# Kernel optimization log

Measured on AMD Instinct MI355X. Metric: run time of the kernel, lower is better.

The kernel has to match this reference:

```python
import jax, jax.numpy as jnp
import numpy as np

NH, WS, SS = 8, 7, 3  # num_heads, window_size, shift_size
EPS = 1e-5


def _rel_pos_index(ws):
    coords = np.stack(np.meshgrid(np.arange(ws), np.arange(ws), indexing='ij'))
    coords = coords.reshape(2, -1)                      # [2, L]
    rel = coords[:, :, None] - coords[:, None, :]       # [2, L, L]
    rel = rel.transpose(1, 2, 0) + (ws - 1)
    return rel[..., 0] * (2 * ws - 1) + rel[..., 1]     # [L, L] int


def _attn_mask(H, W, ws, ss):
    # region labels for shifted-window masking (torchvision semantics)
    img = np.zeros((H, W))
    slices = (slice(0, -ws), slice(-ws, -ss), slice(-ss, None))
    cnt = 0
    for hs in slices:
        for wsl in slices:
            img[hs, wsl] = cnt
            cnt += 1
    win = img.reshape(H // ws, ws, W // ws, ws).transpose(0, 2, 1, 3).reshape(-1, ws * ws)
    mask = (win[:, None, :] != win[:, :, None]).astype(np.float32) * (-100.0)
    return mask  # [nWin, L, L]


def _layernorm(x, gamma, beta):
    mu = jnp.mean(x, axis=-1, keepdims=True)
    var = jnp.mean(jnp.square(x - mu), axis=-1, keepdims=True)
    return (x - mu) * jax.lax.rsqrt(var + EPS) * gamma + beta


def _swin_attention(x, qkv_w, qkv_b, proj_w, proj_b, rpb_table):
    B, H, W, C = x.shape
    HD = C // NH
    L = WS * WS
    nH, nW = H // WS, W // WS
    # cyclic shift
    xs = jnp.roll(x, shift=(-SS, -SS), axis=(1, 2))
    # window partition -> [B*nWin, L, C]
    xw = xs.reshape(B, nH, WS, nW, WS, C).transpose(0, 1, 3, 2, 4, 5).reshape(B * nH * nW, L, C)
    qkv = jnp.einsum('nlc,dc->nld', xw, qkv_w) + qkv_b
    qkv = qkv.reshape(-1, L, 3, NH, HD).transpose(2, 0, 3, 1, 4)  # [3, N, h, L, d]
    q, k, v = qkv[0] * (HD ** -0.5), qkv[1], qkv[2]
    attn = jnp.einsum('nhid,nhjd->nhij', q, k)  # [N, h, L, L]
    bias = rpb_table[jnp.asarray(_rel_pos_index(WS))]  # [L, L, h]
    attn = attn + bias.transpose(2, 0, 1)[None]
    mask = jnp.asarray(_attn_mask(H, W, WS, SS))  # [nWin, L, L]
    nwin = nH * nW
    attn = attn.reshape(B, nwin, NH, L, L) + mask[None, :, None]
    attn = jax.nn.softmax(attn.reshape(-1, NH, L, L), axis=-1)
    out = jnp.einsum('nhij,nhjd->nhid', attn, v).transpose(0, 2, 1, 3).reshape(-1, L, C)
    out = jnp.einsum('nlc,dc->nld', out, proj_w) + proj_b
    # reverse windows and shift
    out = out.reshape(B, nH, nW, WS, WS, C).transpose(0, 1, 3, 2, 4, 5).reshape(B, H, W, C)
    return jnp.roll(out, shift=(SS, SS), axis=(1, 2))


def setup_inputs() -> dict:
    key = jax.random.key(0)
    ks = jax.random.split(key, 8)
    B, H, W, C = 32, 56, 56, 256
    F = 4 * C
    s = 0.02
    return {
        'x': jax.random.normal(ks[0], (B, H, W, C), jnp.float32),
        'qkv_w': jax.random.normal(ks[1], (3 * C, C), jnp.float32) * s,
        'qkv_b': jnp.zeros((3 * C,), jnp.float32),
        'proj_w': jax.random.normal(ks[2], (C, C), jnp.float32) * s,
        'proj_b': jnp.zeros((C,), jnp.float32),
        'rpb_table': jax.random.normal(ks[3], ((2 * WS - 1) ** 2, NH), jnp.float32) * s,
        'gamma1': jnp.ones((C,), jnp.float32),
        'beta1': jnp.zeros((C,), jnp.float32),
        'w1': jax.random.normal(ks[4], (C, F), jnp.float32) * s,
        'b1': jax.random.normal(ks[5], (F,), jnp.float32) * 1e-6,
        'w2': jax.random.normal(ks[6], (F, C), jnp.float32) * s,
        'b2': jax.random.normal(ks[7], (C,), jnp.float32) * 1e-6,
        'gamma2': jnp.ones((C,), jnp.float32),
        'beta2': jnp.zeros((C,), jnp.float32),
    }


def reference(x, qkv_w, qkv_b, proj_w, proj_b, rpb_table, gamma1, beta1, w1, b1, w2, b2, gamma2, beta2):
    # post-norm residual block: x + norm1(attn(x)); x + norm2(mlp(x))
    a = _swin_attention(x, qkv_w, qkv_b, proj_w, proj_b, rpb_table)
    x = x + _layernorm(a, gamma1, beta1)
    h = jax.nn.gelu(jnp.einsum('bhwc,cf->bhwf', x, w1) + b1, approximate=False)
    m = jnp.einsum('bhwf,fc->bhwc', h, w2) + b2
    x = x + _layernorm(m, gamma2, beta2)
    return x
```

## Files before the change

### kernel.cpp

```cpp
#include <hip/hip_runtime.h>
#include <hip/hip_bf16.h>


typedef unsigned short ushort_t;
typedef short bf16x8 __attribute__((ext_vector_type(8)));
typedef float f32x4 __attribute__((ext_vector_type(4)));

#define WAITV0 asm volatile("s_waitcnt vmcnt(0)" ::: "memory")
#define BAR    __builtin_amdgcn_s_barrier()

__device__ __forceinline__ float bf2f(unsigned short u) {
    union { unsigned int i; float f; } x; x.i = ((unsigned int)u) << 16; return x.f;
}
__device__ __forceinline__ unsigned short f2bf(float f) {
    union { float f; unsigned int i; } x; x.f = f;
    unsigned int r = x.i + 0x7fffu + ((x.i >> 16) & 1u);
    return (unsigned short)(r >> 16);
}
__device__ __forceinline__ bf16x8 pack8(float4 a, float4 b) {
    bf16x8 r;
    r[0] = (short)f2bf(a.x); r[1] = (short)f2bf(a.y);
    r[2] = (short)f2bf(a.z); r[3] = (short)f2bf(a.w);
    r[4] = (short)f2bf(b.x); r[5] = (short)f2bf(b.y);
    r[6] = (short)f2bf(b.z); r[7] = (short)f2bf(b.w);
    return r;
}
__device__ __forceinline__ void gl_lds16(const ushort_t* g, ushort_t* l) {
    __builtin_amdgcn_global_load_lds((const __attribute__((address_space(1))) void*)g,
                                     (__attribute__((address_space(3))) void*)l, 16, 0, 0);
}
__device__ __forceinline__ float gelu_f(float v) {
    float s = v * 0.70710678118654752f;
    float ax = fabsf(s);
    float t = __builtin_amdgcn_rcpf(1.0f + 0.3275911f * ax);
    float poly = ((((1.061405429f * t - 1.453152027f) * t + 1.421413741f) * t
                   - 0.284496736f) * t + 0.254829592f) * t;
    float y = 1.0f - poly * __expf(-ax * ax);
    float e = (s < 0.f) ? -y : y;
    return 0.5f * v * (1.0f + e);
}

__device__ __forceinline__ long swin_src_off(int m) {
    int n = m / 49, l = m - n * 49;
    int b = n >> 6, win = n & 63;
    int wh = win >> 3, ww = win & 7;
    int i = l / 7, j = l - i * 7;
    int hs = wh * 7 + i + 3; if (hs >= 56) hs -= 56;
    int ws = ww * 7 + j + 3; if (ws >= 56) ws -= 56;
    return ((long)(b * 56 + hs) * 56 + ws) * 256;
}

__global__ __launch_bounds__(256)
void xgather(const float* __restrict__ x, ushort_t* __restrict__ xg)
{
    int t = blockIdx.x * 256 + threadIdx.x;
    int row = t >> 5, ch = (t & 31) * 8;
    const float* src = x + swin_src_off(row) + ch;
    *(bf16x8*)(xg + (long)row * 256 + ch) = pack8(*(const float4*)src, *(const float4*)(src + 4));
}

template<int SRCT>
__global__ __launch_bounds__(256)
void convW(const float* __restrict__ src, ushort_t* __restrict__ dst, int N, int kshift)
{
    int idx = blockIdx.x * 256 + threadIdx.x;
    int kk = idx & ((1 << kshift) - 1), nn = idx >> kshift;
    float v = SRCT ? src[(long)kk * N + nn] : src[idx];
    dst[idx] = f2bf(v);
}

template<int ACT, int NCOLS>
__global__ __launch_bounds__(256)
void gemm128(const ushort_t* __restrict__ A, const ushort_t* __restrict__ W,
             const float* __restrict__ bias, ushort_t* __restrict__ C,
             int M, int N, int K)
{
    __shared__ ushort_t As[2][128 * 32];
    __shared__ ushort_t Bs[2][128 * 32];
    const int t = threadIdx.x, lane = t & 63, wave = t >> 6;
    const int cpx = gridDim.x >> 3;
    const int wg = (blockIdx.x & 7) * cpx + (blockIdx.x >> 3);
    const int row0 = (wg / NCOLS) * 128, col0 = (wg % NCOLS) * 128;
    const int wm = (wave >> 1) * 64, wn = (wave & 1) * 64;

    const int u0 = t, u1 = t + 256;
    const int r0 = u0 >> 2, s0 = ((u0 & 3) ^ ((r0 >> 1) & 3)) * 8;
    const int r1 = u1 >> 2, s1 = ((u1 & 3) ^ ((r1 >> 1) & 3)) * 8;
    const ushort_t* a0 = A + (long)(row0 + r0) * K + s0;
    const ushort_t* a1 = A + (long)(row0 + r1) * K + s1;
    const ushort_t* b0 = W + (long)(col0 + r0) * K + s0;
    const ushort_t* b1 = W + (long)(col0 + r1) * K + s1;

    int offA[4], offB[4];
    #pragma unroll
    for (int i = 0; i < 4; i++) {
        int ra = wm + i * 16 + (lane & 15);
        offA[i] = ra * 32 + (((lane >> 4) ^ ((ra >> 1) & 3)) * 8);
        int rb = wn + i * 16 + (lane & 15);
        offB[i] = rb * 32 + (((lane >> 4) ^ ((rb >> 1) & 3)) * 8);
    }

    f32x4 acc[4][4] = {};
    gl_lds16(a0, &As[0][u0 * 8]); gl_lds16(a1, &As[0][u1 * 8]);
    gl_lds16(b0, &Bs[0][u0 * 8]); gl_lds16(b1, &Bs[0][u1 * 8]);
    WAITV0; BAR;
    const int nk = K >> 5;
    for (int kt = 0; kt < nk - 1; kt++) {
        const int cur = kt & 1, nxt = cur ^ 1, k1 = (kt + 1) * 32;
        gl_lds16(a0 + k1, &As[nxt][u0 * 8]); gl_lds16(a1 + k1, &As[nxt][u1 * 8]);
        gl_lds16(b0 + k1, &Bs[nxt][u0 * 8]); gl_lds16(b1 + k1, &Bs[nxt][u1 * 8]);
        bf16x8 af[4], bw[4];
        #pragma unroll
        for (int i = 0; i < 4; i++) {
            af[i] = *(const bf16x8*)&As[cur][offA[i]];
            bw[i] = *(const bf16x8*)&Bs[cur][offB[i]];
        }
        #pragma unroll
        for (int mi = 0; mi < 4; mi++)
            #pragma unroll
            for (int ni = 0; ni < 4; ni++)
                acc[mi][ni] = __builtin_amdgcn_mfma_f32_16x16x32_bf16(af[mi], bw[ni], acc[mi][ni], 0, 0, 0);
        WAITV0; BAR;
    }
    {
        const int cur = (nk - 1) & 1;
        bf16x8 af[4], bw[4];
        #pragma unroll
        for (int i = 0; i < 4; i++) {
            af[i] = *(const bf16x8*)&As[cur][offA[i]];
            bw[i] = *(const bf16x8*)&Bs[cur][offB[i]];
        }
        #pragma unroll
        for (int mi = 0; mi < 4; mi++)
            #pragma unroll
            for (int ni = 0; ni < 4; ni++)
                acc[mi][ni] = __builtin_amdgcn_mfma_f32_16x16x32_bf16(af[mi], bw[ni], acc[mi][ni], 0, 0, 0);
    }
    #pragma unroll
    for (int mi = 0; mi < 4; mi++)
        #pragma unroll
        for (int ni = 0; ni < 4; ni++) {
            const int c = col0 + wn + ni * 16 + (lane & 15);
            const float bv = bias[c];
            #pragma unroll
            for (int r = 0; r < 4; r++) {
                const int rr = row0 + wm + mi * 16 + (lane >> 4) * 4 + r;
                float v = acc[mi][ni][r] + bv;
                if (ACT) v = gelu_f(v);
                C[(long)rr * N + c] = f2bf(v);
            }
        }
}

__global__ __launch_bounds__(64)
void attn_mfma(const ushort_t* __restrict__ qkv, const float* __restrict__ rpb,
               ushort_t* __restrict__ out)
{
    __shared__ ushort_t v_t[32 * 72];
    __shared__ ushort_t p_lds[64 * 72];
    __shared__ float bias_s[169];

    const int blk = blockIdx.x;
    const int n = blk >> 3, h = blk & 7;
    const int l = threadIdx.x;
    const long wbase = (long)n * 49 * 768 + h * 32;
    const float scale = 0.17677669529663687f;

    {
        int j = min(l, 48);
        const ushort_t* vr = qkv + wbase + (long)j * 768 + 512;
        #pragma unroll
        for (int c = 0; c < 4; c++) {
            bf16x8 vv = *(const bf16x8*)(vr + c * 8);
            #pragma unroll
            for (int e = 0; e < 8; e++) v_t[(c * 8 + e) * 72 + l] = (ushort_t)vv[e];
        }
    }
    for (int idx = l; idx < 169; idx += 64) bias_s[idx] = rpb[idx * 8 + h];
    __syncthreads();

    f32x4 s[4][4] = {};
    {
        bf16x8 aq[4], bk[4];
        #pragma unroll
        for (int mt = 0; mt < 4; mt++) {
            int i = min(mt * 16 + (l & 15), 48);
            aq[mt] = *(const bf16x8*)(qkv + wbase + (long)i * 768 + (l >> 4) * 8);
        }
        #pragma unroll
        for (int nt = 0; nt < 4; nt++) {
            int j = min(nt * 16 + (l & 15), 48);
            bk[nt] = *(const bf16x8*)(qkv + wbase + (long)j * 768 + 256 + (l >> 4) * 8);
        }
        #pragma unroll
        for (int mt = 0; mt < 4; mt++)
            #pragma unroll
            for (int nt = 0; nt < 4; nt++)
                s[mt][nt] = __builtin_amdgcn_mfma_f32_16x16x32_bf16(aq[mt], bk[nt], s[mt][nt], 0, 0, 0);
    }

    const int win = n & 63, wh = win >> 3, ww = win & 7;
    int yj[4], xj[4], regj[4]; bool jv[4];
    #pragma unroll
    for (int nt = 0; nt < 4; nt++) {
        int j = nt * 16 + (l & 15);
        jv[nt] = (j <= 48);
        int jc = min(j, 48);
        yj[nt] = jc / 7; xj[nt] = jc - yj[nt] * 7;
        int hs = wh * 7 + yj[nt], wsx = ww * 7 + xj[nt];
        regj[nt] = (hs < 49 ? 0 : (hs < 53 ? 1 : 2)) * 3 + (wsx < 49 ? 0 : (wsx < 53 ? 1 : 2));
    }
    float rinv[4][4];
    #pragma unroll
    for (int mt = 0; mt < 4; mt++) {
        #pragma unroll
        for (int r = 0; r < 4; r++) {
            int i = mt * 16 + (l >> 4) * 4 + r;
            int ic = min(i, 48);
            int yi = ic / 7, xi = ic - yi * 7;
            int hs = wh * 7 + yi, wsx = ww * 7 + xi;
            int regi = (hs < 49 ? 0 : (hs < 53 ? 1 : 2)) * 3 + (wsx < 49 ? 0 : (wsx < 53 ? 1 : 2));
            float val[4];
            #pragma unroll
            for (int nt = 0; nt < 4; nt++) {
                float v = s[mt][nt][r] * scale + bias_s[(yi - yj[nt] + 6) * 13 + (xi - xj[nt] + 6)];
                if (regi != regj[nt]) v -= 100.f;
                val[nt] = jv[nt] ? v : -1e30f;
            }
            float mx = fmaxf(fmaxf(val[0], val[1]), fmaxf(val[2], val[3]));
            #pragma unroll
            for (int off = 1; off <= 8; off <<= 1) mx = fmaxf(mx, __shfl_xor(mx, off));
            float sum = 0.f;
            #pragma unroll
            for (int nt = 0; nt < 4; nt++) { val[nt] = __expf(val[nt] - mx); sum += val[nt]; }
            #pragma unroll
            for (int off = 1; off <= 8; off <<= 1) sum += __shfl_xor(sum, off);
            rinv[mt][r] = 1.0f / sum;
            #pragma unroll
            for (int nt = 0; nt < 4; nt++)
                p_lds[i * 72 + nt * 16 + (l & 15)] = f2bf(val[nt]);
        }
    }
    __syncthreads();

    f32x4 o[4][2] = {};
    #pragma unroll
    for (int ks = 0; ks < 2; ks++) {
        bf16x8 pa[4], vb[2];
        #pragma unroll
        for (int mt = 0; mt < 4; mt++)
            pa[mt] = *(const bf16x8*)&p_lds[(mt * 16 + (l & 15)) * 72 + ks * 32 + (l >> 4) * 8];
        #pragma unroll
        for (int nt = 0; nt < 2; nt++)
            vb[nt] = *(const bf16x8*)&v_t[(nt * 16 + (l & 15)) * 72 + ks * 32 + (l >> 4) * 8];
        #pragma unroll
        for (int mt = 0; mt < 4; mt++)
            #pragma unroll
            for (int nt = 0; nt < 2; nt++)
                o[mt][nt] = __builtin_amdgcn_mfma_f32_16x16x32_bf16(pa[mt], vb[nt], o[mt][nt], 0, 0, 0);
    }
    #pragma unroll
    for (int mt = 0; mt < 4; mt++)
        #pragma unroll
        for (int r = 0; r < 4; r++) {
            int i = mt * 16 + (l >> 4) * 4 + r;
            if (i < 49) {
                float rs = rinv[mt][r];
                #pragma unroll
                for (int nt = 0; nt < 2; nt++) {
                    int d = nt * 16 + (l & 15);
                    out[((long)n * 49 + i) * 256 + h * 32 + d] = f2bf(o[mt][nt][r] * rs);
                }
            }
        }
}

__global__ __launch_bounds__(512)
void projln1(const ushort_t* __restrict__ A, const ushort_t* __restrict__ W,
             const float* __restrict__ pb, const float* __restrict__ x,
             const float* __restrict__ gamma, const float* __restrict__ beta,
             ushort_t* __restrict__ x1b)
{
    __shared__ ushort_t As[2][128 * 32];
    __shared__ ushort_t Bs[2][256 * 32];
    __shared__ float red_s[128][4];
    __shared__ float red_ss[128][4];
    __shared__ int srow_s[128];
    const int t = threadIdx.x, lane = t & 63, w = t >> 6;
    const int row0 = blockIdx.x * 128;
    const int wm = (w >> 2) * 64, wn = (w & 3) * 64;

    if (t < 128) srow_s[t] = (int)(swin_src_off(row0 + t) >> 8);

    const int ra0 = t >> 2, sa0 = ((t & 3) ^ ((ra0 >> 1) & 3)) * 8;
    const ushort_t* ag = A + (long)(row0 + ra0) * 256 + sa0;
    const int ub0 = t, ub1 = t + 512;
    const int rb0 = ub0 >> 2, sb0 = ((ub0 & 3) ^ ((rb0 >> 1) & 3)) * 8;
    const int rb1 = ub1 >> 2, sb1 = ((ub1 & 3) ^ ((rb1 >> 1) & 3)) * 8;
    const ushort_t* bg0 = W + (long)rb0 * 256 + sb0;
    const ushort_t* bg1 = W + (long)rb1 * 256 + sb1;

    int offA[4], offB[4];
    #pragma unroll
    for (int i = 0; i < 4; i++) {
        int ra = wm + i * 16 + (lane & 15);
        offA[i] = ra * 32 + (((lane >> 4) ^ ((ra >> 1) & 3)) * 8);
        int rb = wn + i * 16 + (lane & 15);
        offB[i] = rb * 32 + (((lane >> 4) ^ ((rb >> 1) & 3)) * 8);
    }

    f32x4 acc[4][4] = {};
    gl_lds16(ag, &As[0][t * 8]);
    gl_lds16(bg0, &Bs[0][ub0 * 8]); gl_lds16(bg1, &Bs[0][ub1 * 8]);
    WAITV0; BAR;
    for (int kt = 0; kt < 7; kt++) {
        const int cur = kt & 1, nxt = cur ^ 1, k1 = (kt + 1) * 32;
        gl_lds16(ag + k1, &As[nxt][t * 8]);
        gl_lds16(bg0 + k1, &Bs[nxt][ub0 * 8]); gl_lds16(bg1 + k1, &Bs[nxt][ub1 * 8]);
        bf16x8 af[4], bw[4];
        #pragma unroll
        for (int i = 0; i < 4; i++) {
            af[i] = *(const bf16x8*)&As[cur][offA[i]];
            bw[i] = *(const bf16x8*)&Bs[cur][offB[i]];
        }
        #pragma unroll
        for (int mi = 0; mi < 4; mi++)
            #pragma unroll
            for (int ni = 0; ni < 4; ni++)
                acc[mi][ni] = __builtin_amdgcn_mfma_f32_16x16x32_bf16(af[mi], bw[ni], acc[mi][ni], 0, 0, 0);
        WAITV0; BAR;
    }
    {
        bf16x8 af[4], bw[4];
        #pragma unroll
        for (int i = 0; i < 4; i++) {
            af[i] = *(const bf16x8*)&As[1][offA[i]];
            bw[i] = *(const bf16x8*)&Bs[1][offB[i]];
        }
        #pragma unroll
        for (int mi = 0; mi < 4; mi++)
            #pragma unroll
            for (int ni = 0; ni < 4; ni++)
                acc[mi][ni] = __builtin_amdgcn_mfma_f32_16x16x32_bf16(af[mi], bw[ni], acc[mi][ni], 0, 0, 0);
    }

    float pbv[4], g1v[4], be1v[4];
    #pragma unroll
    for (int ni = 0; ni < 4; ni++) {
        int col = wn + ni * 16 + (lane & 15);
        pbv[ni] = pb[col]; g1v[ni] = gamma[col]; be1v[ni] = beta[col];
    }
    #pragma unroll
    for (int mi = 0; mi < 4; mi++)
        #pragma unroll
        for (int rr = 0; rr < 4; rr++) {
            float s = 0.f, ss = 0.f;
            #pragma unroll
            for (int ni = 0; ni < 4; ni++) {
                float v = acc[mi][ni][rr] + pbv[ni];
                acc[mi][ni][rr] = v; s += v; ss += v * v;
            }
            #pragma unroll
            for (int off = 1; off <= 8; off <<= 1) { s += __shfl_xor(s, off); ss += __shfl_xor(ss, off); }
            if ((lane & 15) == 0) {
                int r = wm + mi * 16 + (lane >> 4) * 4 + rr;
                red_s[r][w & 3] = s; red_ss[r][w & 3] = ss;
            }
        }
    __syncthreads();
    #pragma unroll
    for (int mi = 0; mi < 4; mi++)
        #pragma unroll
        for (int rr = 0; rr < 4; rr++) {
            const int r = wm + mi * 16 + (lane >> 4) * 4 + rr;
            const float s = red_s[r][0] + red_s[r][1] + red_s[r][2] + red_s[r][3];
            const float ss = red_ss[r][0] + red_ss[r][1] + red_ss[r][2] + red_ss[r][3];
            const float mu = s * (1.0f / 256.0f);
            const float rstd = rsqrtf(ss * (1.0f / 256.0f) - mu * mu + 1e-5f);
            const long sp = srow_s[r];
            #pragma unroll
            for (int ni = 0; ni < 4; ni++) {
                int col = wn + ni * 16 + (lane & 15);
                float o = x[sp * 256 + col] + (acc[mi][ni][rr] - mu) * rstd * g1v[ni] + be1v[ni];
                x1b[sp * 256 + col] = f2bf(o);
            }
        }
}

__global__ __launch_bounds__(256)
void mlp2ln2(const ushort_t* __restrict__ A, const ushort_t* __restrict__ W,
             const float* __restrict__ pb, const ushort_t* __restrict__ x1res,
             const float* __restrict__ gamma, const float* __restrict__ beta,
             float* __restrict__ out)
{
    __shared__ ushort_t As[2][64 * 32];
    __shared__ ushort_t Bs[2][256 * 32];
    __shared__ float red_s[64][4];
    __shared__ float red_ss[64][4];
    const int t = threadIdx.x, lane = t & 63, w = t >> 6;
    const int row0 = blockIdx.x * 64;
    const int wn = w * 64;

    const int ra0 = t >> 2, sa0 = ((t & 3) ^ ((ra0 >> 1) & 3)) * 8;
    const ushort_t* ag = A + (long)(row0 + ra0) * 1024 + sa0;
    const ushort_t* bg[4];
    int ub[4];
    #pragma unroll
    for (int i = 0; i < 4; i++) {
        ub[i] = t + i * 256;
        int rb = ub[i] >> 2, sb = ((ub[i] & 3) ^ ((rb >> 1) & 3)) * 8;
        bg[i] = W + (long)rb * 1024 + sb;
    }

    int offA[4], offB[4];
    #pragma unroll
    for (int i = 0; i < 4; i++) {
        int ra = i * 16 + (lane & 15);
        offA[i] = ra * 32 + (((lane >> 4) ^ ((ra >> 1) & 3)) * 8);
        int rb = wn + i * 16 + (lane & 15);
        offB[i] = rb * 32 + (((lane >> 4) ^ ((rb >> 1) & 3)) * 8);
    }

    f32x4 acc[4][4] = {};
    gl_lds16(ag, &As[0][t * 8]);
    #pragma unroll
    for (int i = 0; i < 4; i++) gl_lds16(bg[i], &Bs[0][ub[i] * 8]);
    WAITV0; BAR;
    for (int kt = 0; kt < 31; kt++) {
        const int cur = kt & 1, nxt = cur ^ 1, k1 = (kt + 1) * 32;
        gl_lds16(ag + k1, &As[nxt][t * 8]);
        #pragma unroll
        for (int i = 0; i < 4; i++) gl_lds16(bg[i] + k1, &Bs[nxt][ub[i] * 8]);
        bf16x8 af[4], bw[4];
        #pragma unroll
        for (int i2 = 0; i2 < 4; i2++) {
            af[i2] = *(const bf16x8*)&As[cur][offA[i2]];
            bw[i2] = *(const bf16x8*)&Bs[cur][offB[i2]];
        }
        #pragma unroll
        for (int mi = 0; mi < 4; mi++)
            #pragma unroll
            for (int ni = 0; ni < 4; ni++)
                acc[mi][ni] = __builtin_amdgcn_mfma_f32_16x16x32_bf16(af[mi], bw[ni], acc[mi][ni], 0, 0, 0);
        WAITV0; BAR;
    }
    {
        bf16x8 af[4], bw[4];
        #pragma unroll
        for (int i2 = 0; i2 < 4; i2++) {
            af[i2] = *(const bf16x8*)&As[1][offA[i2]];
            bw[i2] = *(const bf16x8*)&Bs[1][offB[i2]];
        }
        #pragma unroll
        for (int mi = 0; mi < 4; mi++)
            #pragma unroll
            for (int ni = 0; ni < 4; ni++)
                acc[mi][ni] = __builtin_amdgcn_mfma_f32_16x16x32_bf16(af[mi], bw[ni], acc[mi][ni], 0, 0, 0);
    }
    float pbv[4], g2v[4], be2v[4];
    #pragma unroll
    for (int ni = 0; ni < 4; ni++) {
        int col = wn + ni * 16 + (lane & 15);
        pbv[ni] = pb[col]; g2v[ni] = gamma[col]; be2v[ni] = beta[col];
    }
    #pragma unroll
    for (int mi = 0; mi < 4; mi++)
        #pragma unroll
        for (int rr = 0; rr < 4; rr++) {
            float s = 0.f, ss = 0.f;
            #pragma unroll
            for (int ni = 0; ni < 4; ni++) {
                float v = acc[mi][ni][rr] + pbv[ni];
                acc[mi][ni][rr] = v; s += v; ss += v * v;
            }
            #pragma unroll
            for (int off = 1; off <= 8; off <<= 1) { s += __shfl_xor(s, off); ss += __shfl_xor(ss, off); }
            if ((lane & 15) == 0) {
                int r = mi * 16 + (lane >> 4) * 4 + rr;
                red_s[r][w] = s; red_ss[r][w] = ss;
            }
        }
    __syncthreads();
    #pragma unroll
    for (int mi = 0; mi < 4; mi++)
        #pragma unroll
        for (int rr = 0; rr < 4; rr++) {
            const int r = mi * 16 + (lane >> 4) * 4 + rr;
            const float s = red_s[r][0] + red_s[r][1] + red_s[r][2] + red_s[r][3];
            const float ss = red_ss[r][0] + red_ss[r][1] + red_ss[r][2] + red_ss[r][3];
            const float mu = s * (1.0f / 256.0f);
            const float rstd = rsqrtf(ss * (1.0f / 256.0f) - mu * mu + 1e-5f);
            const long gr = row0 + r;
            #pragma unroll
            for (int ni = 0; ni < 4; ni++) {
                int col = wn + ni * 16 + (lane & 15);
                out[gr * 256 + col] = bf2f(x1res[gr * 256 + col])
                                    + (acc[mi][ni][rr] - mu) * rstd * g2v[ni] + be2v[ni];
            }
        }
}

extern "C" void kernel_launch(void* const* d_in, const int* in_sizes, int n_in,
                              void* d_out, int out_size, void* d_ws, size_t ws_size,
                              hipStream_t stream) {
    const float* x      = (const float*)d_in[0];
    const float* qkv_w  = (const float*)d_in[1];
    const float* qkv_b  = (const float*)d_in[2];
    const float* proj_w = (const float*)d_in[3];
    const float* proj_b = (const float*)d_in[4];
    const float* rpb    = (const float*)d_in[5];
    const float* gamma1 = (const float*)d_in[6];
    const float* beta1  = (const float*)d_in[7];
    const float* w1     = (const float*)d_in[8];
    const float* b1     = (const float*)d_in[9];
    const float* w2     = (const float*)d_in[10];
    const float* b2     = (const float*)d_in[11];
    const float* gamma2 = (const float*)d_in[12];
    const float* beta2  = (const float*)d_in[13];
    float* outf = (float*)d_out;

    char* ob = (char*)d_out;
    ushort_t* xg      = (ushort_t*)ob;
    ushort_t* attnout = (ushort_t*)(ob + 51380224ULL);

    char* ws = (char*)d_ws;
    ushort_t* qkvb  = (ushort_t*)ws;
    ushort_t* hbuf  = (ushort_t*)ws;
    ushort_t* x1b   = (ushort_t*)(ws + 154140672ULL);
    ushort_t* wqkvb = (ushort_t*)(ws + 205520896ULL);
    ushort_t* wprojb= (ushort_t*)(ws + 205914112ULL);
    ushort_t* w1t   = (ushort_t*)(ws + 206045184ULL);
    ushort_t* w2t   = (ushort_t*)(ws + 206569472ULL);

    const int M = 100352, MC = 50176;
    dim3 blk(256);
    xgather<<<dim3(M / 8), blk, 0, stream>>>(x, xg);
    convW<0><<<dim3(768),  blk, 0, stream>>>(qkv_w,  wqkvb,  768,  8);
    convW<0><<<dim3(256),  blk, 0, stream>>>(proj_w, wprojb, 256,  8);
    convW<1><<<dim3(1024), blk, 0, stream>>>(w1,     w1t,    1024, 8);
    convW<1><<<dim3(1024), blk, 0, stream>>>(w2,     w2t,    256, 10);
    gemm128<0, 6><<<dim3(4704), blk, 0, stream>>>(xg, wqkvb, qkv_b, qkvb, M, 768, 256);
    attn_mfma<<<dim3(16384), dim3(64), 0, stream>>>(qkvb, rpb, attnout);
    projln1<<<dim3(784), dim3(512), 0, stream>>>(attnout, wprojb, proj_b, x,
                                                 gamma1, beta1, x1b);
    for (int c2 = 0; c2 < 2; c2++) {
        const long off = (long)c2 * MC * 256;
        gemm128<1, 8><<<dim3(3136), blk, 0, stream>>>(x1b + off, w1t, b1, hbuf, MC, 1024, 256);
        mlp2ln2<<<dim3(784), blk, 0, stream>>>(hbuf, w2t, b2, x1b + off,
                                               gamma2, beta2, outf + off);
    }
}
```

Before: 547.0 us.

## Fuse shifted-window gather into QKV GEMM and widen GEMM tiles to 128x256

Removes the separate xgather kernel. The QKV GEMM now reads fp32 x directly through the shifted-window index map, converts it to bf16 in registers and stores it to LDS, which avoids writing and re-reading an intermediate buffer. The GEMM is also generalised to 512-thread blocks with a 128x256 output tile and used for both the QKV and MLP1 GEMMs, giving more B-tile reuse per block. In exchange, the fused A path uses register-staged loads instead of direct global-to-LDS copies, and the larger tile lowers block count and occupancy.

```diff
diff --git a/kernel.cpp b/kernel.cpp
--- a/kernel.cpp
+++ b/kernel.cpp
@@ -7,6 +7,7 @@
 typedef float f32x4 __attribute__((ext_vector_type(4)));
 
 #define WAITV0 asm volatile("s_waitcnt vmcnt(0)" ::: "memory")
+#define WAITL0 asm volatile("s_waitcnt lgkmcnt(0)" ::: "memory")
 #define BAR    __builtin_amdgcn_s_barrier()
 
 __device__ __forceinline__ float bf2f(unsigned short u) {
@@ -50,15 +51,6 @@
     return ((long)(b * 56 + hs) * 56 + ws) * 256;
 }
 
-__global__ __launch_bounds__(256)
-void xgather(const float* __restrict__ x, ushort_t* __restrict__ xg)
-{
-    int t = blockIdx.x * 256 + threadIdx.x;
-    int row = t >> 5, ch = (t & 31) * 8;
-    const float* src = x + swin_src_off(row) + ch;
-    *(bf16x8*)(xg + (long)row * 256 + ch) = pack8(*(const float4*)src, *(const float4*)(src + 4));
-}
-
 template<int SRCT>
 __global__ __launch_bounds__(256)
 void convW(const float* __restrict__ src, ushort_t* __restrict__ dst, int N, int kshift)
@@ -69,46 +61,64 @@
     dst[idx] = f2bf(v);
 }
 
-template<int ACT, int NCOLS>
-__global__ __launch_bounds__(256)
-void gemm128(const ushort_t* __restrict__ A, const ushort_t* __restrict__ W,
-             const float* __restrict__ bias, ushort_t* __restrict__ C,
-             int M, int N, int K)
+template<int ACT, int AMODE, int NCOLS>
+__global__ __launch_bounds__(512)
+void gemmW(const void* __restrict__ Av, const ushort_t* __restrict__ W,
+           const float* __restrict__ bias, ushort_t* __restrict__ C,
+           int M, int N, int K)
 {
     __shared__ ushort_t As[2][128 * 32];
-    __shared__ ushort_t Bs[2][128 * 32];
-    const int t = threadIdx.x, lane = t & 63, wave = t >> 6;
+    __shared__ ushort_t Bs[2][256 * 32];
+    const int t = threadIdx.x, lane = t & 63, w = t >> 6;
     const int cpx = gridDim.x >> 3;
     const int wg = (blockIdx.x & 7) * cpx + (blockIdx.x >> 3);
-    const int row0 = (wg / NCOLS) * 128, col0 = (wg % NCOLS) * 128;
-    const int wm = (wave >> 1) * 64, wn = (wave & 1) * 64;
-
-    const int u0 = t, u1 = t + 256;
-    const int r0 = u0 >> 2, s0 = ((u0 & 3) ^ ((r0 >> 1) & 3)) * 8;
-    const int r1 = u1 >> 2, s1 = ((u1 & 3) ^ ((r1 >> 1) & 3)) * 8;
-    const ushort_t* a0 = A + (long)(row0 + r0) * K + s0;
-    const ushort_t* a1 = A + (long)(row0 + r1) * K + s1;
-    const ushort_t* b0 = W + (long)(col0 + r0) * K + s0;
-    const ushort_t* b1 = W + (long)(col0 + r1) * K + s1;
+    const int row0 = (wg / NCOLS) * 128, col0 = (wg % NCOLS) * 256;
+    const int wm = (w >> 2) * 64, wn = (w & 3) * 64;
+
+    const int ra = t >> 2, sa = ((t & 3) ^ ((ra >> 1) & 3)) * 8;
+    const ushort_t* ag = nullptr;
+    const float* axr = nullptr;
+    if (AMODE == 0) ag = (const ushort_t*)Av + (long)(row0 + ra) * K + sa;
+    else            axr = (const float*)Av + swin_src_off(row0 + ra) + sa;
+
+    const int ub0 = t, ub1 = t + 512;
+    const int rb0 = ub0 >> 2, sb0 = ((ub0 & 3) ^ ((rb0 >> 1) & 3)) * 8;
+    const int rb1 = ub1 >> 2, sb1 = ((ub1 & 3) ^ ((rb1 >> 1) & 3)) * 8;
+    const ushort_t* bg0 = W + (long)(col0 + rb0) * K + sb0;
+    const ushort_t* bg1 = W + (long)(col0 + rb1) * K + sb1;
 
     int offA[4], offB[4];
     #pragma unroll
     for (int i = 0; i < 4; i++) {
-        int ra = wm + i * 16 + (lane & 15);
-        offA[i] = ra * 32 + (((lane >> 4) ^ ((ra >> 1) & 3)) * 8);
-        int rb = wn + i * 16 + (lane & 15);
-        offB[i] = rb * 32 + (((lane >> 4) ^ ((rb >> 1) & 3)) * 8);
+        int r2 = wm + i * 16 + (lane & 15);
+        offA[i] = r2 * 32 + (((lane >> 4) ^ ((r2 >> 1) & 3)) * 8);
+        int r3 = wn + i * 16 + (lane & 15);
+        offB[i] = r3 * 32 + (((lane >> 4) ^ ((r3 >> 1) & 3)) * 8);
     }
 
     f32x4 acc[4][4] = {};
-    gl_lds16(a0, &As[0][u0 * 8]); gl_lds16(a1, &As[0][u1 * 8]);
-    gl_lds16(b0, &Bs[0][u0 * 8]); gl_lds16(b1, &Bs[0][u1 * 8]);
-    WAITV0; BAR;
+    if (AMODE == 0) {
+        gl_lds16(ag, &As[0][t * 8]);
+    } else {
+        float4 va = *(const float4*)axr, vb = *(const float4*)(axr + 4);
+        *(bf16x8*)&As[0][t * 8] = pack8(va, vb);
+    }
+    gl_lds16(bg0, &Bs[0][ub0 * 8]);
+    gl_lds16(bg1, &Bs[0][ub1 * 8]);
+    WAITV0; if (AMODE == 1) { WAITL0; } BAR;
+
     const int nk = K >> 5;
     for (int kt = 0; kt < nk - 1; kt++) {
         const int cur = kt & 1, nxt = cur ^ 1, k1 = (kt + 1) * 32;
-        gl_lds16(a0 + k1, &As[nxt][u0 * 8]); gl_lds16(a1 + k1, &As[nxt][u1 * 8]);
-        gl_lds16(b0 + k1, &Bs[nxt][u0 * 8]); gl_lds16(b1 + k1, &Bs[nxt][u1 * 8]);
+        float4 va, vb;
+        if (AMODE == 1) {
+            va = *(const float4*)(axr + k1);
+            vb = *(const float4*)(axr + k1 + 4);
+        } else {
+            gl_lds16(ag + k1, &As[nxt][t * 8]);
+        }
+        gl_lds16(bg0 + k1, &Bs[nxt][ub0 * 8]);
+        gl_lds16(bg1 + k1, &Bs[nxt][ub1 * 8]);
         bf16x8 af[4], bw[4];
         #pragma unroll
         for (int i = 0; i < 4; i++) {
@@ -120,7 +130,9 @@
             #pragma unroll
             for (int ni = 0; ni < 4; ni++)
                 acc[mi][ni] = __builtin_amdgcn_mfma_f32_16x16x32_bf16(af[mi], bw[ni], acc[mi][ni], 0, 0, 0);
-        WAITV0; BAR;
+        if (AMODE == 1)
+            *(bf16x8*)&As[nxt][t * 8] = pack8(va, vb);
+        WAITV0; if (AMODE == 1) { WAITL0; } BAR;
     }
     {
         const int cur = (nk - 1) & 1;
@@ -519,9 +531,7 @@
     const float* beta2  = (const float*)d_in[13];
     float* outf = (float*)d_out;
 
-    char* ob = (char*)d_out;
-    ushort_t* xg      = (ushort_t*)ob;
-    ushort_t* attnout = (ushort_t*)(ob + 51380224ULL);
+    ushort_t* attnout = (ushort_t*)d_out;
 
     char* ws = (char*)d_ws;
     ushort_t* qkvb  = (ushort_t*)ws;
@@ -534,18 +544,17 @@
 
     const int M = 100352, MC = 50176;
     dim3 blk(256);
-    xgather<<<dim3(M / 8), blk, 0, stream>>>(x, xg);
     convW<0><<<dim3(768),  blk, 0, stream>>>(qkv_w,  wqkvb,  768,  8);
     convW<0><<<dim3(256),  blk, 0, stream>>>(proj_w, wprojb, 256,  8);
     convW<1><<<dim3(1024), blk, 0, stream>>>(w1,     w1t,    1024, 8);
     convW<1><<<dim3(1024), blk, 0, stream>>>(w2,     w2t,    256, 10);
-    gemm128<0, 6><<<dim3(4704), blk, 0, stream>>>(xg, wqkvb, qkv_b, qkvb, M, 768, 256);
+    gemmW<0, 1, 3><<<dim3(2352), dim3(512), 0, stream>>>(x, wqkvb, qkv_b, qkvb, M, 768, 256);
     attn_mfma<<<dim3(16384), dim3(64), 0, stream>>>(qkvb, rpb, attnout);
     projln1<<<dim3(784), dim3(512), 0, stream>>>(attnout, wprojb, proj_b, x,
                                                  gamma1, beta1, x1b);
     for (int c2 = 0; c2 < 2; c2++) {
         const long off = (long)c2 * MC * 256;
-        gemm128<1, 8><<<dim3(3136), blk, 0, stream>>>(x1b + off, w1t, b1, hbuf, MC, 1024, 256);
+        gemmW<1, 0, 4><<<dim3(1568), dim3(512), 0, stream>>>(x1b + off, w1t, b1, hbuf, MC, 1024, 256);
         mlp2ln2<<<dim3(784), blk, 0, stream>>>(hbuf, w2t, b2, x1b + off,
                                                gamma2, beta2, outf + off);
     }
```

Result: no change. 537.7 us (-1.7%).
